# Performance work log

Measured on AMD Instinct MI355X. Metric: run time of the kernel, lower is better.

The kernel has to match this reference:

```python
import jax, jax.numpy as jnp
import numpy as np

NUM_HEADS = 16


def setup_inputs() -> dict:
    key = jax.random.key(0)
    k1, k2, k3 = jax.random.split(key, 3)
    T, B, E = 2048, 2, 1024
    x = jax.random.normal(k1, (T, B, E), dtype=jnp.float32)
    in_proj_w = jax.random.normal(k2, (E, 3 * E), dtype=jnp.float32) * (E ** -0.5)
    in_proj_b = jnp.zeros((3 * E,), dtype=jnp.float32)
    out_w = jax.random.normal(k3, (E, E), dtype=jnp.float32) * (E ** -0.5)
    out_b = jnp.zeros((E,), dtype=jnp.float32)
    return {"x": x, "in_proj_w": in_proj_w, "in_proj_b": in_proj_b,
            "out_w": out_w, "out_b": out_b}


def reference(x, in_proj_w, in_proj_b, out_w, out_b):
    # x: (tgt_len, bsz, embed_dim) -- seq-first, self-attention (q is k is v)
    T, B, E = x.shape
    H = NUM_HEADS
    D = E // H
    scaling = D ** -0.5
    # packed in-projection: einsum('bne,ef->bnf') over (T,B,E)
    proj = jnp.einsum('tbe,ef->tbf', x, in_proj_w) + in_proj_b
    q, k, v = jnp.split(proj, 3, axis=-1)  # each (T, B, E)
    # reshape to (T, B*H, D) then transpose to (B*H, T, D)
    q = q.reshape(T, B * H, D).transpose(1, 0, 2)
    k = k.reshape(T, B * H, D).transpose(1, 0, 2)
    v = v.reshape(T, B * H, D).transpose(1, 0, 2)
    # full O(T^2) attention matrix, scaling applied after QK^T as in source
    attn = jnp.einsum('bie,bje->bij', q, k) * scaling  # (B*H, T, T)
    attn = jax.nn.softmax(attn, axis=-1)
    out = jnp.einsum('bij,bje->bie', attn, v)  # (B*H, T, D)
    # faithful to source: reshape directly (no head transpose-back)
    out = out.reshape(B, T, E)
    out = jnp.einsum('bte,ef->btf', out, out_w) + out_b
    return out
```

## Files before the change

kernel.cpp:

```cpp
#include <hip/hip_runtime.h>
#include <stdint.h>

#define TSEQ 2048
#define NB 2
#define EMB 1024
#define NHEAD 16
#define HDIM 64
#define KSPLIT 2
#define NT (TSEQ / KSPLIT / 64)
#define QSCALE 0.18033688f

typedef __bf16 bf16x8 __attribute__((ext_vector_type(8)));
typedef __bf16 bf16x4 __attribute__((ext_vector_type(4)));
typedef float f32x4 __attribute__((ext_vector_type(4)));
typedef float f32x16 __attribute__((ext_vector_type(16)));
typedef unsigned int u32x4 __attribute__((ext_vector_type(4)));

__device__ __forceinline__ void gload_lds16(const void* g, void* lds) {
    __builtin_amdgcn_global_load_lds(
        (const __attribute__((address_space(1))) unsigned int*)g,
        (__attribute__((address_space(3))) unsigned int*)lds, 16, 0, 0);
}

__device__ __forceinline__ float fast_exp2(float x) {
#if __has_builtin(__builtin_amdgcn_exp2f)
    return __builtin_amdgcn_exp2f(x);
#else
    return exp2f(x);
#endif
}

__device__ __forceinline__ unsigned cvt_pk_bf16(float lo, float hi) {
    unsigned r;
    asm("v_cvt_pk_bf16_f32 %0, %1, %2" : "=v"(r) : "v"(lo), "v"(hi));
    return r;
}

__device__ __forceinline__ void swap32(unsigned& a, unsigned& b) {
    asm("v_permlane32_swap_b32 %0, %1" : "+v"(a), "+v"(b));
}

__device__ __forceinline__ bf16x8 as_bf16x8(u32x4 u) {
    union { u32x4 u; bf16x8 h; } c;
    c.u = u;
    return c.h;
}

__global__ __launch_bounds__(256) void prep_kernel(
    const float* __restrict__ x, const float* __restrict__ w_in,
    const float* __restrict__ w_out,
    __bf16* __restrict__ xb, __bf16* __restrict__ wiT, __bf16* __restrict__ whT)
{
    __shared__ float tile[32][33];
    int bid = blockIdx.x;
    const int tid = threadIdx.x;
    if (bid < 4096) {
        const size_t idx = ((size_t)bid * 256 + tid) * 4;
        float4 v = *(const float4*)(x + idx);
        bf16x4 o = { (__bf16)v.x, (__bf16)v.y, (__bf16)v.z, (__bf16)v.w };
        *(bf16x4*)(xb + idx) = o;
        return;
    }
    bid -= 4096;
    int bx = bid & 127;
    const int by = bid >> 7;
    const float* src; __bf16* dst; int sn;
    if (bx < 96) { src = w_in;  dst = wiT; sn = 3072; }
    else         { bx -= 96; src = w_out; dst = whT; sn = 1024; }
    const int tx = tid & 31, ty = tid >> 5;
    #pragma unroll
    for (int i = 0; i < 4; ++i)
        tile[ty + i * 8][tx] = src[(size_t)(by * 32 + ty + i * 8) * sn + bx * 32 + tx];
    __syncthreads();
    #pragma unroll
    for (int i = 0; i < 4; ++i) {
        float v = tile[tx][ty + i * 8];
        dst[(size_t)(bx * 32 + ty + i * 8) * 1024 + by * 32 + tx] = (__bf16)v;
    }
}

__global__ __launch_bounds__(256) void gemm_qkv_kernel(
    const __bf16* __restrict__ A, const __bf16* __restrict__ BT,
    const float* __restrict__ bias,
    __bf16* __restrict__ Oq, __bf16* __restrict__ Ok, __bf16* __restrict__ Ov)
{
    __shared__ __align__(16) __bf16 As[128 * 64];
    __shared__ __align__(16) __bf16 Bs[128 * 64];
    const int tid = threadIdx.x;
    const int wave = tid >> 6, lane = tid & 63;
    const int l16 = lane & 15, quad = lane >> 4;
    const int wm = wave >> 1, wn = wave & 1;
    const int m0 = blockIdx.y * 128, n0 = blockIdx.x * 128;

    f32x4 acc[4][4];
    #pragma unroll
    for (int mt = 0; mt < 4; ++mt)
        #pragma unroll
        for (int nt = 0; nt < 4; ++nt)
            #pragma unroll
            for (int r = 0; r < 4; ++r) acc[mt][nt][r] = 0.f;

    int smrow[4], schunk[4], sbase[4];
    #pragma unroll
    for (int i = 0; i < 4; ++i) {
        int linear = (wave * 4 + i) * 64 + lane;
        smrow[i] = linear >> 3;
        schunk[i] = (linear & 7) ^ (smrow[i] & 7);
        sbase[i] = (wave * 4 + i) * 512;
    }

    for (int k0 = 0; k0 < 1024; k0 += 64) {
        #pragma unroll
        for (int i = 0; i < 4; ++i) {
            gload_lds16(A + (size_t)(m0 + smrow[i]) * 1024 + k0 + schunk[i] * 8,
                        As + sbase[i]);
            gload_lds16(BT + (size_t)(n0 + smrow[i]) * 1024 + k0 + schunk[i] * 8,
                        Bs + sbase[i]);
        }
        __syncthreads();
        #pragma unroll
        for (int kk = 0; kk < 2; ++kk) {
            bf16x8 am[4], bn[4];
            #pragma unroll
            for (int mt = 0; mt < 4; ++mt) {
                int row = wm * 64 + mt * 16 + l16;
                int c = (kk * 4 + quad) ^ (row & 7);
                am[mt] = *(const bf16x8*)(As + row * 64 + c * 8);
            }
            #pragma unroll
            for (int nt = 0; nt < 4; ++nt) {
                int row = wn * 64 + nt * 16 + l16;
                int c = (kk * 4 + quad) ^ (row & 7);
                bn[nt] = *(const bf16x8*)(Bs + row * 64 + c * 8);
            }
            #pragma unroll
            for (int mt = 0; mt < 4; ++mt)
                #pragma unroll
                for (int nt = 0; nt < 4; ++nt)
                    acc[mt][nt] = __builtin_amdgcn_mfma_f32_16x16x32_bf16(
                        am[mt], bn[nt], acc[mt][nt], 0, 0, 0);
        }
        __syncthreads();
    }

    #pragma unroll
    for (int nt = 0; nt < 4; ++nt) {
        const int col = n0 + wn * 64 + nt * 16 + l16;
        const float bv = bias[col];
        const int sec = col >> 10, f = col & 1023;
        const int h = f >> 6, d = f & 63;
        #pragma unroll
        for (int mt = 0; mt < 4; ++mt)
            #pragma unroll
            for (int r = 0; r < 4; ++r) {
                const int row = m0 + wm * 64 + mt * 16 + quad * 4 + r;
                float v = acc[mt][nt][r] + bv;
                const int t = row >> 1, b = row & 1;
                const int bh = b * NHEAD + h;
                const size_t idx = ((size_t)bh * TSEQ + t) * HDIM + d;
                if (sec == 0)
                    Oq[idx] = (__bf16)(v * QSCALE);
                else if (sec == 1)
                    Ok[idx] = (__bf16)v;
                else
                    Ov[idx] = (__bf16)v;
            }
    }
}

__global__ __launch_bounds__(256) void vtrans_kernel(
    const __bf16* __restrict__ V, __bf16* __restrict__ Vt)
{
    __shared__ __bf16 T[64 * 67];
    const int bh = blockIdx.y;
    const int t0 = blockIdx.x * 64;
    const int tid = threadIdx.x;
    const int r = tid >> 2;
    const int c = (tid & 3) * 16;
    const __bf16* src = V + ((size_t)bh * TSEQ + t0 + r) * HDIM + c;
    bf16x8 a = *(const bf16x8*)src;
    bf16x8 b = *(const bf16x8*)(src + 8);
    #pragma unroll
    for (int j = 0; j < 8; ++j) {
        T[r * 67 + c + j] = a[j];
        T[r * 67 + c + 8 + j] = b[j];
    }
    __syncthreads();
    const int dr = tid >> 2;
    const int tc = (tid & 3) * 16;
    bf16x8 o0, o1;
    #pragma unroll
    for (int j = 0; j < 8; ++j) {
        o0[j] = T[(tc + j) * 67 + dr];
        o1[j] = T[(tc + 8 + j) * 67 + dr];
    }
    __bf16* dst = Vt + ((size_t)bh * HDIM + dr) * TSEQ + t0 + tc;
    *(bf16x8*)dst = o0;
    *(bf16x8*)(dst + 8) = o1;
}

__global__ __launch_bounds__(256, 2) void attn_mfma_kernel(
    const __bf16* __restrict__ Q, const __bf16* __restrict__ K,
    const __bf16* __restrict__ Vt,
    __bf16* __restrict__ O0, __bf16* __restrict__ O1,
    float* __restrict__ L0, float* __restrict__ L1)
{
    __shared__ __align__(16) __bf16 Ks[2][64 * 64];
    __shared__ __align__(16) __bf16 Vs[2][64 * 64];

    const int tid  = threadIdx.x;
    const int wave = tid >> 6;
    const int lane = tid & 63;
    const int l31  = lane & 31;
    const int hi   = lane >> 5;
    const int m7   = l31 & 7;

    const int lid = blockIdx.x;
    const int xcd = lid & 7;
    const int j   = lid >> 3;
    const int grp = xcd * 8 + (j >> 3);
    const int qb  = j & 7;
    const int bh  = grp >> 1;
    const int z   = grp & 1;

    const int q0   = qb * 256 + wave * 64;
    const int kbase0 = z * (TSEQ / KSPLIT);

    __bf16* __restrict__ Opart = (z == 0) ? O0 : O1;
    float*  __restrict__ Lpart = (z == 0) ? L0 : L1;

    bf16x8 qf[2][4];
    #pragma unroll
    for (int g = 0; g < 2; ++g) {
        const __bf16* Qrow =
            Q + ((size_t)bh * TSEQ + q0 + g * 32 + l31) * HDIM + 8 * hi;
        #pragma unroll
        for (int c = 0; c < 4; ++c)
            qf[g][c] = *(const bf16x8*)(Qrow + 16 * c);
    }

    f32x16 Oacc[2][2];
    #pragma unroll
    for (int g = 0; g < 2; ++g)
        #pragma unroll
        for (int dt = 0; dt < 2; ++dt)
            #pragma unroll
            for (int r = 0; r < 16; ++r) Oacc[g][dt][r] = 0.f;
    float l4[2][4] = {{0.f, 0.f, 0.f, 0.f}, {0.f, 0.f, 0.f, 0.f}};

    const __bf16* Kbase = K + ((size_t)bh * TSEQ + kbase0) * HDIM;
    const __bf16* Vbase = Vt + (size_t)bh * HDIM * TSEQ + kbase0;

    int srow[2], schk[2];
    #pragma unroll
    for (int i = 0; i < 2; ++i) {
        const int s = wave * 2 + i;
        srow[i] = s * 8 + (lane >> 3);
        schk[i] = (lane & 7) ^ (srow[i] & 7);
    }

#define STAGE(buf, kt)                                                        \
    {                                                                         \
        _Pragma("unroll")                                                     \
        for (int i = 0; i < 2; ++i) {                                         \
            const int s = wave * 2 + i;                                       \
            gload_lds16(Kbase + (size_t)((kt) * 64 + srow[i]) * HDIM          \
                            + schk[i] * 8,                                    \
                        &Ks[buf][s * 512]);                                   \
            gload_lds16(Vbase + (size_t)srow[i] * TSEQ + (kt) * 64            \
                            + schk[i] * 8,                                    \
                        &Vs[buf][s * 512]);                                   \
        }                                                                     \
    }

#define SOFTMAX(sa, g, s)                                                     \
    {                                                                         \
        float p[16];                                                          \
        _Pragma("unroll")                                                     \
        for (int r = 0; r < 16; ++r) {                                        \
            p[r] = fast_exp2((sa)[r]);                                        \
            l4[g][r & 3] += p[r];                                             \
        }                                                                     \
        unsigned x[8];                                                        \
        _Pragma("unroll")                                                     \
        for (int i = 0; i < 8; ++i)                                           \
            x[i] = cvt_pk_bf16(p[2 * i], p[2 * i + 1]);                       \
        swap32(x[0], x[2]); swap32(x[1], x[3]);                               \
        swap32(x[4], x[6]); swap32(x[5], x[7]);                               \
        pa[g][2 * (s)][0] = x[0]; pa[g][2 * (s)][1] = x[1];                   \
        pa[g][2 * (s)][2] = x[2]; pa[g][2 * (s)][3] = x[3];                   \
        pa[g][2 * (s) + 1][0] = x[4]; pa[g][2 * (s) + 1][1] = x[5];           \
        pa[g][2 * (s) + 1][2] = x[6]; pa[g][2 * (s) + 1][3] = x[7];           \
    }

    STAGE(0, 0);

    for (int kt = 0; kt < NT; ++kt) {
        const int b = kt & 1;
        __syncthreads();
        if (kt + 1 < NT) STAGE(b ^ 1, kt + 1);

        u32x4 pa[2][4];
        #pragma unroll
        for (int s = 0; s < 2; ++s) {
            f32x16 sa0, sa1;
            #pragma unroll
            for (int r = 0; r < 16; ++r) { sa0[r] = 0.f; sa1[r] = 0.f; }
            #pragma unroll
            for (int c = 0; c < 4; ++c) {
                bf16x8 kf = *(const bf16x8*)(
                    &Ks[b][(32 * s + l31) * 64 + (((c << 1) | hi) ^ m7) * 8]);
                sa0 = __builtin_amdgcn_mfma_f32_32x32x16_bf16(
                    kf, qf[0][c], sa0, 0, 0, 0);
                sa1 = __builtin_amdgcn_mfma_f32_32x32x16_bf16(
                    kf, qf[1][c], sa1, 0, 0, 0);
            }
            SOFTMAX(sa0, 0, s);
            SOFTMAX(sa1, 1, s);
        }

        #pragma unroll
        for (int dt = 0; dt < 2; ++dt)
            #pragma unroll
            for (int ks = 0; ks < 4; ++ks) {
                bf16x8 vf = *(const bf16x8*)(
                    &Vs[b][(dt * 32 + l31) * 64 + (((ks << 1) | hi) ^ m7) * 8]);
                Oacc[0][dt] = __builtin_amdgcn_mfma_f32_32x32x16_bf16(
                    as_bf16x8(pa[0][ks]), vf, Oacc[0][dt], 0, 0, 0);
                Oacc[1][dt] = __builtin_amdgcn_mfma_f32_32x32x16_bf16(
                    as_bf16x8(pa[1][ks]), vf, Oacc[1][dt], 0, 0, 0);
            }
    }
#undef STAGE
#undef SOFTMAX

    #pragma unroll
    for (int g = 0; g < 2; ++g) {
        float v = (l4[g][0] + l4[g][1]) + (l4[g][2] + l4[g][3]);
        v += __shfl_xor(v, 32);
        if (hi == 0)
            Lpart[(size_t)bh * TSEQ + q0 + g * 32 + l31] = v;
    }

    const size_t base = ((size_t)bh * TSEQ + q0) * HDIM;
    #pragma unroll
    for (int g = 0; g < 2; ++g)
        #pragma unroll
        for (int dt = 0; dt < 2; ++dt)
            #pragma unroll
            for (int r = 0; r < 16; ++r) {
                const int q = g * 32 + (r & 3) + 8 * (r >> 2) + 4 * hi;
                Opart[base + (size_t)q * HDIM + dt * 32 + l31] =
                    (__bf16)Oacc[g][dt][r];
            }
}

__global__ __launch_bounds__(256) void normalize_kernel(
    const __bf16* __restrict__ O0, const __bf16* __restrict__ O1,
    const float* __restrict__ L0, const float* __restrict__ L1,
    __bf16* __restrict__ Ob)
{
    const size_t gid = (size_t)blockIdx.x * 256 + threadIdx.x;
    const size_t idx = gid * 8;
    const size_t qi = idx >> 6;
    const float inv = 1.f / (L0[qi] + L1[qi]);
    bf16x8 a = *(const bf16x8*)(O0 + idx);
    bf16x8 b = *(const bf16x8*)(O1 + idx);
    bf16x8 o;
    #pragma unroll
    for (int j = 0; j < 8; ++j)
        o[j] = (__bf16)(((float)a[j] + (float)b[j]) * inv);
    *(bf16x8*)(Ob + idx) = o;
}

__global__ __launch_bounds__(256) void gemm_out_kernel(
    const __bf16* __restrict__ A, const __bf16* __restrict__ BT,
    const float* __restrict__ bias, float* __restrict__ out)
{
    __shared__ __align__(16) __bf16 As[128 * 64];
    __shared__ __align__(16) __bf16 Bs[128 * 64];
    const int tid = threadIdx.x;
    const int wave = tid >> 6, lane = tid & 63;
    const int l16 = lane & 15, quad = lane >> 4;
    const int wm = wave >> 1, wn = wave & 1;
    const int m0 = blockIdx.y * 128, n0 = blockIdx.x * 128;

    f32x4 acc[4][4];
    #pragma unroll
    for (int mt = 0; mt < 4; ++mt)
        #pragma unroll
        for (int nt = 0; nt < 4; ++nt)
            #pragma unroll
            for (int r = 0; r < 4; ++r) acc[mt][nt][r] = 0.f;

    int smrow[4], schunk[4], sbase[4];
    #pragma unroll
    for (int i = 0; i < 4; ++i) {
        int linear = (wave * 4 + i) * 64 + lane;
        smrow[i] = linear >> 3;
        schunk[i] = (linear & 7) ^ (smrow[i] & 7);
        sbase[i] = (wave * 4 + i) * 512;
    }

    for (int k0 = 0; k0 < 1024; k0 += 64) {
        #pragma unroll
        for (int i = 0; i < 4; ++i) {
            gload_lds16(A + (size_t)(m0 + smrow[i]) * 1024 + k0 + schunk[i] * 8,
                        As + sbase[i]);
            gload_lds16(BT + (size_t)(n0 + smrow[i]) * 1024 + k0 + schunk[i] * 8,
                        Bs + sbase[i]);
        }
        __syncthreads();
        #pragma unroll
        for (int kk = 0; kk < 2; ++kk) {
            bf16x8 am[4], bn[4];
            #pragma unroll
            for (int mt = 0; mt < 4; ++mt) {
                int row = wm * 64 + mt * 16 + l16;
                int c = (kk * 4 + quad) ^ (row & 7);
                am[mt] = *(const bf16x8*)(As + row * 64 + c * 8);
            }
            #pragma unroll
            for (int nt = 0; nt < 4; ++nt) {
                int row = wn * 64 + nt * 16 + l16;
                int c = (kk * 4 + quad) ^ (row & 7);
                bn[nt] = *(const bf16x8*)(Bs + row * 64 + c * 8);
            }
            #pragma unroll
            for (int mt = 0; mt < 4; ++mt)
                #pragma unroll
                for (int nt = 0; nt < 4; ++nt)
                    acc[mt][nt] = __builtin_amdgcn_mfma_f32_16x16x32_bf16(
                        am[mt], bn[nt], acc[mt][nt], 0, 0, 0);
        }
        __syncthreads();
    }

    #pragma unroll
    for (int nt = 0; nt < 4; ++nt) {
        const int col = n0 + wn * 64 + nt * 16 + l16;
        const float bv = bias[col];
        #pragma unroll
        for (int mt = 0; mt < 4; ++mt)
            #pragma unroll
            for (int r = 0; r < 4; ++r) {
                const int row = m0 + wm * 64 + mt * 16 + quad * 4 + r;
                out[(size_t)row * 1024 + col] = acc[mt][nt][r] + bv;
            }
    }
}

extern "C" void kernel_launch(void* const* d_in, const int* in_sizes, int n_in,
                              void* d_out, int out_size, void* d_ws, size_t ws_size,
                              hipStream_t stream) {
    const float* x     = (const float*)d_in[0];
    const float* w_in  = (const float*)d_in[1];
    const float* b_in  = (const float*)d_in[2];
    const float* w_out = (const float*)d_in[3];
    const float* b_out = (const float*)d_in[4];
    float* out = (float*)d_out;

    const size_t M1 = (size_t)1024 * 1024;
    __bf16* ws  = (__bf16*)d_ws;
    __bf16* xb  = ws;
    __bf16* wiT = xb  + 4 * M1;
    __bf16* whT = wiT + 3 * M1;
    __bf16* Qb  = whT + 1 * M1;
    __bf16* Kb  = Qb  + 4 * M1;
    __bf16* Vt  = Kb  + 4 * M1;
    __bf16* O0  = Vt  + 4 * M1;
    __bf16* O1  = O0  + 4 * M1;
    float*  L0  = (float*)(O1 + 4 * M1);
    float*  L1  = L0 + 65536;
    __bf16* Vb  = (__bf16*)d_out;
    __bf16* Ob  = xb;

    prep_kernel<<<8192, 256, 0, stream>>>(x, w_in, w_out, xb, wiT, whT);
    gemm_qkv_kernel<<<dim3(24, 32), 256, 0, stream>>>(
        xb, wiT, b_in, Qb, Kb, Vb);
    vtrans_kernel<<<dim3(32, 32), 256, 0, stream>>>(Vb, Vt);
    attn_mfma_kernel<<<dim3(512), 256, 0, stream>>>(
        Qb, Kb, Vt, O0, O1, L0, L1);
    normalize_kernel<<<2048, 256, 0, stream>>>(
        O0, O1, L0, L1, Ob);
    gemm_out_kernel<<<dim3(8, 32), 256, 0, stream>>>(
        Ob, whT, b_out, out);
}
```

Measured before the change: 195.3 us.

## Drop split-K attention, fuse normalization, and shrink output GEMM tiles

Removes the two-way split of the key dimension in attention, so each block processes the full sequence and normalizes its output in-kernel using the per-row sum held in shared memory. This eliminates the separate normalize kernel and the partial O/L buffers. The output projection GEMM moves from 128x128 to 64x64 tiles, launching four times as many blocks. The cost is half as many attention blocks (256 on a large GPU), which lowers parallelism and lengthens per-block latency, and the smaller GEMM tiles get less data reuse.

Result: slower. 199.5 us (+2.2%).

```diff
diff --git a/kernel.cpp b/kernel.cpp
--- a/kernel.cpp
+++ b/kernel.cpp
@@ -6,8 +6,7 @@
 #define EMB 1024
 #define NHEAD 16
 #define HDIM 64
-#define KSPLIT 2
-#define NT (TSEQ / KSPLIT / 64)
+#define NT (TSEQ / 64)
 #define QSCALE 0.18033688f
 
 typedef __bf16 bf16x8 __attribute__((ext_vector_type(8)));
@@ -201,12 +200,11 @@
 
 __global__ __launch_bounds__(256, 2) void attn_mfma_kernel(
     const __bf16* __restrict__ Q, const __bf16* __restrict__ K,
-    const __bf16* __restrict__ Vt,
-    __bf16* __restrict__ O0, __bf16* __restrict__ O1,
-    float* __restrict__ L0, float* __restrict__ L1)
+    const __bf16* __restrict__ Vt, __bf16* __restrict__ Ob)
 {
     __shared__ __align__(16) __bf16 Ks[2][64 * 64];
     __shared__ __align__(16) __bf16 Vs[2][64 * 64];
+    __shared__ float Linv[4][64];
 
     const int tid  = threadIdx.x;
     const int wave = tid >> 6;
@@ -218,16 +216,10 @@
     const int lid = blockIdx.x;
     const int xcd = lid & 7;
     const int j   = lid >> 3;
-    const int grp = xcd * 8 + (j >> 3);
+    const int bh  = xcd * 4 + (j >> 3);
     const int qb  = j & 7;
-    const int bh  = grp >> 1;
-    const int z   = grp & 1;
-
-    const int q0   = qb * 256 + wave * 64;
-    const int kbase0 = z * (TSEQ / KSPLIT);
-
-    __bf16* __restrict__ Opart = (z == 0) ? O0 : O1;
-    float*  __restrict__ Lpart = (z == 0) ? L0 : L1;
+
+    const int q0 = qb * 256 + wave * 64;
 
     bf16x8 qf[2][4];
     #pragma unroll
@@ -248,8 +240,8 @@
             for (int r = 0; r < 16; ++r) Oacc[g][dt][r] = 0.f;
     float l4[2][4] = {{0.f, 0.f, 0.f, 0.f}, {0.f, 0.f, 0.f, 0.f}};
 
-    const __bf16* Kbase = K + ((size_t)bh * TSEQ + kbase0) * HDIM;
-    const __bf16* Vbase = Vt + (size_t)bh * HDIM * TSEQ + kbase0;
+    const __bf16* Kbase = K + (size_t)bh * TSEQ * HDIM;
+    const __bf16* Vbase = Vt + (size_t)bh * HDIM * TSEQ;
 
     int srow[2], schk[2];
     #pragma unroll
@@ -339,8 +331,9 @@
         float v = (l4[g][0] + l4[g][1]) + (l4[g][2] + l4[g][3]);
         v += __shfl_xor(v, 32);
         if (hi == 0)
-            Lpart[(size_t)bh * TSEQ + q0 + g * 32 + l31] = v;
-    }
+            Linv[wave][g * 32 + l31] = 1.f / v;
+    }
+    __syncthreads();
 
     const size_t base = ((size_t)bh * TSEQ + q0) * HDIM;
     #pragma unroll
@@ -349,87 +342,70 @@
         for (int dt = 0; dt < 2; ++dt)
             #pragma unroll
             for (int r = 0; r < 16; ++r) {
-                const int q = g * 32 + (r & 3) + 8 * (r >> 2) + 4 * hi;
-                Opart[base + (size_t)q * HDIM + dt * 32 + l31] =
-                    (__bf16)Oacc[g][dt][r];
-            }
-}
-
-__global__ __launch_bounds__(256) void normalize_kernel(
-    const __bf16* __restrict__ O0, const __bf16* __restrict__ O1,
-    const float* __restrict__ L0, const float* __restrict__ L1,
-    __bf16* __restrict__ Ob)
-{
-    const size_t gid = (size_t)blockIdx.x * 256 + threadIdx.x;
-    const size_t idx = gid * 8;
-    const size_t qi = idx >> 6;
-    const float inv = 1.f / (L0[qi] + L1[qi]);
-    bf16x8 a = *(const bf16x8*)(O0 + idx);
-    bf16x8 b = *(const bf16x8*)(O1 + idx);
-    bf16x8 o;
-    #pragma unroll
-    for (int j = 0; j < 8; ++j)
-        o[j] = (__bf16)(((float)a[j] + (float)b[j]) * inv);
-    *(bf16x8*)(Ob + idx) = o;
+                const int ql = g * 32 + (r & 3) + 8 * (r >> 2) + 4 * hi;
+                const float inv = Linv[wave][ql];
+                Ob[base + (size_t)ql * HDIM + dt * 32 + l31] =
+                    (__bf16)(Oacc[g][dt][r] * inv);
+            }
 }
 
 __global__ __launch_bounds__(256) void gemm_out_kernel(
     const __bf16* __restrict__ A, const __bf16* __restrict__ BT,
     const float* __restrict__ bias, float* __restrict__ out)
 {
-    __shared__ __align__(16) __bf16 As[128 * 64];
-    __shared__ __align__(16) __bf16 Bs[128 * 64];
+    __shared__ __align__(16) __bf16 As[64 * 64];
+    __shared__ __align__(16) __bf16 Bs[64 * 64];
     const int tid = threadIdx.x;
     const int wave = tid >> 6, lane = tid & 63;
     const int l16 = lane & 15, quad = lane >> 4;
     const int wm = wave >> 1, wn = wave & 1;
-    const int m0 = blockIdx.y * 128, n0 = blockIdx.x * 128;
-
-    f32x4 acc[4][4];
-    #pragma unroll
-    for (int mt = 0; mt < 4; ++mt)
-        #pragma unroll
-        for (int nt = 0; nt < 4; ++nt)
+    const int m0 = blockIdx.y * 64, n0 = blockIdx.x * 64;
+
+    f32x4 acc[2][2];
+    #pragma unroll
+    for (int mt = 0; mt < 2; ++mt)
+        #pragma unroll
+        for (int nt = 0; nt < 2; ++nt)
             #pragma unroll
             for (int r = 0; r < 4; ++r) acc[mt][nt][r] = 0.f;
 
-    int smrow[4], schunk[4], sbase[4];
-    #pragma unroll
-    for (int i = 0; i < 4; ++i) {
-        int linear = (wave * 4 + i) * 64 + lane;
-        smrow[i] = linear >> 3;
-        schunk[i] = (linear & 7) ^ (smrow[i] & 7);
-        sbase[i] = (wave * 4 + i) * 512;
+    int srow[2], schk[2], sbase[2];
+    #pragma unroll
+    for (int i = 0; i < 2; ++i) {
+        const int s = wave * 2 + i;
+        srow[i] = s * 8 + (lane >> 3);
+        schk[i] = (lane & 7) ^ (srow[i] & 7);
+        sbase[i] = s * 512;
     }
 
     for (int k0 = 0; k0 < 1024; k0 += 64) {
         #pragma unroll
-        for (int i = 0; i < 4; ++i) {
-            gload_lds16(A + (size_t)(m0 + smrow[i]) * 1024 + k0 + schunk[i] * 8,
+        for (int i = 0; i < 2; ++i) {
+            gload_lds16(A + (size_t)(m0 + srow[i]) * 1024 + k0 + schk[i] * 8,
                         As + sbase[i]);
-            gload_lds16(BT + (size_t)(n0 + smrow[i]) * 1024 + k0 + schunk[i] * 8,
+            gload_lds16(BT + (size_t)(n0 + srow[i]) * 1024 + k0 + schk[i] * 8,
                         Bs + sbase[i]);
         }
         __syncthreads();
         #pragma unroll
         for (int kk = 0; kk < 2; ++kk) {
-            bf16x8 am[4], bn[4];
-            #pragma unroll
-            for (int mt = 0; mt < 4; ++mt) {
-                int row = wm * 64 + mt * 16 + l16;
+            bf16x8 am[2], bn[2];
+            #pragma unroll
+            for (int mt = 0; mt < 2; ++mt) {
+                int row = wm * 32 + mt * 16 + l16;
                 int c = (kk * 4 + quad) ^ (row & 7);
                 am[mt] = *(const bf16x8*)(As + row * 64 + c * 8);
             }
             #pragma unroll
-            for (int nt = 0; nt < 4; ++nt) {
-                int row = wn * 64 + nt * 16 + l16;
+            for (int nt = 0; nt < 2; ++nt) {
+                int row = wn * 32 + nt * 16 + l16;
                 int c = (kk * 4 + quad) ^ (row & 7);
                 bn[nt] = *(const bf16x8*)(Bs + row * 64 + c * 8);
             }
             #pragma unroll
-            for (int mt = 0; mt < 4; ++mt)
+            for (int mt = 0; mt < 2; ++mt)
                 #pragma unroll
-                for (int nt = 0; nt < 4; ++nt)
+                for (int nt = 0; nt < 2; ++nt)
                     acc[mt][nt] = __builtin_amdgcn_mfma_f32_16x16x32_bf16(
                         am[mt], bn[nt], acc[mt][nt], 0, 0, 0);
         }
@@ -437,14 +413,14 @@
     }
 
     #pragma unroll
-    for (int nt = 0; nt < 4; ++nt) {
-        const int col = n0 + wn * 64 + nt * 16 + l16;
+    for (int nt = 0; nt < 2; ++nt) {
+        const int col = n0 + wn * 32 + nt * 16 + l16;
         const float bv = bias[col];
         #pragma unroll
-        for (int mt = 0; mt < 4; ++mt)
+        for (int mt = 0; mt < 2; ++mt)
             #pragma unroll
             for (int r = 0; r < 4; ++r) {
-                const int row = m0 + wm * 64 + mt * 16 + quad * 4 + r;
+                const int row = m0 + wm * 32 + mt * 16 + quad * 4 + r;
                 out[(size_t)row * 1024 + col] = acc[mt][nt][r] + bv;
             }
     }
@@ -468,10 +444,6 @@
     __bf16* Qb  = whT + 1 * M1;
     __bf16* Kb  = Qb  + 4 * M1;
     __bf16* Vt  = Kb  + 4 * M1;
-    __bf16* O0  = Vt  + 4 * M1;
-    __bf16* O1  = O0  + 4 * M1;
-    float*  L0  = (float*)(O1 + 4 * M1);
-    float*  L1  = L0 + 65536;
     __bf16* Vb  = (__bf16*)d_out;
     __bf16* Ob  = xb;
 
@@ -479,10 +451,8 @@
     gemm_qkv_kernel<<<dim3(24, 32), 256, 0, stream>>>(
         xb, wiT, b_in, Qb, Kb, Vb);
     vtrans_kernel<<<dim3(32, 32), 256, 0, stream>>>(Vb, Vt);
-    attn_mfma_kernel<<<dim3(512), 256, 0, stream>>>(
-        Qb, Kb, Vt, O0, O1, L0, L1);
-    normalize_kernel<<<2048, 256, 0, stream>>>(
-        O0, O1, L0, L1, Ob);
-    gemm_out_kernel<<<dim3(8, 32), 256, 0, stream>>>(
+    attn_mfma_kernel<<<dim3(256), 256, 0, stream>>>(
+        Qb, Kb, Vt, Ob);
+    gemm_out_kernel<<<dim3(16, 64), 256, 0, stream>>>(
         Ob, whT, b_out, out);
 }
```
